# Optimization experiments

Hardware: AMD Instinct MI355X
Metric: run time of the kernel (lower is better)

Reference implementation:

```python
import jax, jax.numpy as jnp
import numpy as np

NUM_HEADS = 4
OUT_DIM = 64
IN_DIM = 128

def setup_inputs() -> dict:
    key = jax.random.key(0)
    k1, k2, k3, k4 = jax.random.split(key, 4)
    h = jax.random.normal(k1, (4, 256, IN_DIM), dtype=jnp.float32)
    adj = jax.random.randint(k2, (4, 256, 256), 0, 2).astype(jnp.int32)
    W = jax.random.normal(k3, (IN_DIM, NUM_HEADS * OUT_DIM), dtype=jnp.float32) * (1.0 / np.sqrt(IN_DIM))
    a = jax.random.normal(k4, (2 * OUT_DIM, 1), dtype=jnp.float32) * 0.1
    return {"h": h, "adj": adj, "W": W, "a": a}

def reference(h, adj, W, a):
    B, N, _ = h.shape
    H, D = NUM_HEADS, OUT_DIM
    Wh = (h @ W).reshape(B, N, H, D)                      # [B,N,H,D]
    # Exact replication of the torch repeat/view construction (row-major, same as torch.view)
    a1 = jnp.tile(Wh, (1, 1, 1, N)).reshape(B, N * H, N, D)
    a2 = jnp.tile(Wh, (1, N, 1, 1)).reshape(B, N * H, N, D)
    a_input = jnp.concatenate([a1, a2], axis=3)           # [B,N*H,N,2D]
    e = jax.nn.leaky_relu((a_input @ a)[..., 0], negative_slope=0.2)
    e = e.reshape(B, H, N, N)
    mask = adj[:, None, :, :] == 0                        # broadcast over heads
    attention = jax.nn.softmax(jnp.where(mask, -jnp.inf, e), axis=3)  # [B,H,N,N]
    h_prime = jnp.einsum('bhij,bjhd->bihd', attention, Wh)             # [B,N,H,D]
    return h_prime.reshape(B, N, H * D)
```

## Files before the change

kernel.cpp:

```cpp
#include <hip/hip_runtime.h>


typedef __attribute__((ext_vector_type(8))) short bf16x8;
typedef __attribute__((ext_vector_type(4))) float f32x4;

__device__ __forceinline__ short bf1(float x) {
  unsigned u = __builtin_bit_cast(unsigned, x);
  u = (u + 0x7FFFu + ((u >> 16) & 1u)) >> 16;
  return (short)u;
}
__device__ __forceinline__ bf16x8 pack8(float4 a, float4 b) {
  bf16x8 r;
  r[0]=bf1(a.x); r[1]=bf1(a.y); r[2]=bf1(a.z); r[3]=bf1(a.w);
  r[4]=bf1(b.x); r[5]=bf1(b.y); r[6]=bf1(b.z); r[7]=bf1(b.w);
  return r;
}

__global__ __launch_bounds__(512) void gat_prep(
    const float* __restrict__ h, const float* __restrict__ W,
    const float* __restrict__ a,
    short* __restrict__ WhT, float* __restrict__ f1g, float* __restrict__ f2g)
{
  const int tid  = threadIdx.x;
  const int lane = tid & 63;
  const int quad = lane >> 4, col = lane & 15;
  const int wv   = tid >> 6;
  const int blk  = blockIdx.x;
  const int nt = blk & 3, mt = (blk >> 2) & 3, b = blk >> 4;

  __shared__ short WbT[64][136];
  __shared__ float f1p[64][4];
  __shared__ float f2p[64][4];

#pragma unroll
  for (int q = 0; q < 4; q++) {
    const int idx = q * 512 + tid;
    const int k = idx >> 4, c4 = idx & 15;
    float4 w4 = *(const float4*)(W + k * 256 + nt * 64 + c4 * 4);
    WbT[c4*4 + 0][k] = bf1(w4.x);
    WbT[c4*4 + 1][k] = bf1(w4.y);
    WbT[c4*4 + 2][k] = bf1(w4.z);
    WbT[c4*4 + 3][k] = bf1(w4.w);
  }
  __syncthreads();

  const int tc = wv & 3;
  const float a1v = a[tc*16 + col];
  const float a2v = a[64 + tc*16 + col];

#pragma unroll
  for (int q = 0; q < 2; q++) {
    const int tr = (wv >> 2) * 2 + q;
    const float* hrow = h + (b*256 + mt*64 + tr*16 + col) * 128 + quad*8;
    f32x4 acc = {0.f, 0.f, 0.f, 0.f};
#pragma unroll
    for (int kk = 0; kk < 4; kk++) {
      float4 lo = *(const float4*)(hrow + kk*32);
      float4 hi = *(const float4*)(hrow + kk*32 + 4);
      bf16x8 bw = *(const bf16x8*)&WbT[tc*16 + col][kk*32 + quad*8];
      acc = __builtin_amdgcn_mfma_f32_16x16x32_bf16(pack8(lo, hi), bw, acc, 0, 0, 0);
    }
    {
      const int dcol = nt*64 + tc*16 + col;
      const int n0   = mt*64 + tr*16 + quad*4;
      int2 pk;
      pk.x = (int)((unsigned)(unsigned short)bf1(acc[0]) |
                   ((unsigned)(unsigned short)bf1(acc[1]) << 16));
      pk.y = (int)((unsigned)(unsigned short)bf1(acc[2]) |
                   ((unsigned)(unsigned short)bf1(acc[3]) << 16));
      *(int2*)(WhT + b*65536 + dcol*256 + n0) = pk;
    }
#pragma unroll
    for (int r = 0; r < 4; r++) {
      float v1 = acc[r] * a1v;
      float v2 = acc[r] * a2v;
#pragma unroll
      for (int off = 1; off < 16; off <<= 1) {
        v1 += __shfl_xor(v1, off, 64);
        v2 += __shfl_xor(v2, off, 64);
      }
      if (col == 0) {
        const int row = tr*16 + quad*4 + r;
        f1p[row][tc] = v1;
        f2p[row][tc] = v2;
      }
    }
  }
  __syncthreads();

  if (tid < 64) {
    const float s = f1p[tid][0] + f1p[tid][1] + f1p[tid][2] + f1p[tid][3];
    f1g[b*1024 + (mt*64 + tid)*4 + nt] = s;
  } else if (tid < 128) {
    const int n = tid - 64;
    const float s = f2p[n][0] + f2p[n][1] + f2p[n][2] + f2p[n][3];
    f2g[b*1024 + (mt*64 + n)*4 + nt] = s;
  }
}

__global__ __launch_bounds__(512) void gat_attn(
    const short* __restrict__ WhT, const float* __restrict__ f1g,
    const float* __restrict__ f2g, const int* __restrict__ adj,
    float* __restrict__ out)
{
  const int tid  = threadIdx.x;
  const int lane = tid & 63;
  const int quad = lane >> 4, col = lane & 15;
  const int wv   = tid >> 6;
  const int blk  = blockIdx.x;
  const int it2 = blk & 7, hp = (blk >> 3) & 3, b = blk >> 5;
  const int i0 = it2 * 32;

  __shared__ short attb[32][264];
  __shared__ float sinv[32];

#pragma unroll
  for (int rq = 0; rq < 4; rq++) {
    const int rr = wv*4 + rq;
    const int i  = i0 + rr;
    const float s1v = f1g[b*1024 + hp*256 + i];
    float4 f2v = *(const float4*)(f2g + b*1024 + (i & 3)*256 + lane*4);
    int4 av = *(const int4*)(adj + (b*256 + i)*256 + lane*4);
    float e0 = s1v + f2v.x, e1 = s1v + f2v.y, e2 = s1v + f2v.z, e3 = s1v + f2v.w;
    e0 = e0 > 0.f ? e0 : 0.2f*e0;  e1 = e1 > 0.f ? e1 : 0.2f*e1;
    e2 = e2 > 0.f ? e2 : 0.2f*e2;  e3 = e3 > 0.f ? e3 : 0.2f*e3;
    e0 = av.x ? e0 : -1e30f;  e1 = av.y ? e1 : -1e30f;
    e2 = av.z ? e2 : -1e30f;  e3 = av.w ? e3 : -1e30f;
    float m = fmaxf(fmaxf(e0, e1), fmaxf(e2, e3));
#pragma unroll
    for (int off = 32; off > 0; off >>= 1) m = fmaxf(m, __shfl_xor(m, off, 64));
    float x0 = __expf(e0 - m), x1 = __expf(e1 - m);
    float x2 = __expf(e2 - m), x3 = __expf(e3 - m);
    float s = (x0 + x1) + (x2 + x3);
    int2 pk2;
    pk2.x = (int)((unsigned)(unsigned short)bf1(x0) |
                  ((unsigned)(unsigned short)bf1(x1) << 16));
    pk2.y = (int)((unsigned)(unsigned short)bf1(x2) |
                  ((unsigned)(unsigned short)bf1(x3) << 16));
    *(int2*)&attb[rr][lane*4] = pk2;
#pragma unroll
    for (int off = 32; off > 0; off >>= 1) s += __shfl_xor(s, off, 64);
    if (lane == 0) sinv[rr] = 1.f / s;
  }
  __syncthreads();

  const int rt = wv >> 2, ct = wv & 3;
  bf16x8 af[8];
#pragma unroll
  for (int kk = 0; kk < 8; kk++)
    af[kk] = *(const bf16x8*)&attb[rt*16 + col][kk*32 + quad*8];
  const short* bp = WhT + b*65536 + (hp*64 + ct*16 + col)*256 + quad*8;
  f32x4 acc = {0.f, 0.f, 0.f, 0.f};
#pragma unroll
  for (int kk = 0; kk < 8; kk++) {
    bf16x8 bv = *(const bf16x8*)(bp + kk*32);
    acc = __builtin_amdgcn_mfma_f32_16x16x32_bf16(af[kk], bv, acc, 0, 0, 0);
  }
#pragma unroll
  for (int r = 0; r < 4; r++) {
    const int m = rt*16 + quad*4 + r;
    out[(b*256 + i0 + m)*256 + hp*64 + ct*16 + col] = acc[r] * sinv[m];
  }
}

extern "C" void kernel_launch(void* const* d_in, const int* in_sizes, int n_in,
                              void* d_out, int out_size, void* d_ws, size_t ws_size,
                              hipStream_t stream) {
  const float* h   = (const float*)d_in[0];
  const int*   adj = (const int*)d_in[1];
  const float* W   = (const float*)d_in[2];
  const float* a   = (const float*)d_in[3];
  float* out = (float*)d_out;

  short* WhT = (short*)d_ws;
  float* f1g = (float*)((char*)d_ws + 4*256*256*2);
  float* f2g = f1g + 4*1024;

  gat_prep<<<64, 512, 0, stream>>>(h, W, a, WhT, f1g, f2g);
  gat_attn<<<128, 512, 0, stream>>>(WhT, f1g, f2g, adj, out);
}
```

Before: 71.96 us.

## Prefetch attention operands, drop softmax max pass, and split prep grid finer

The attention kernel now issues all WhT, adj, f1 and f2 global loads at the start, so their latency overlaps the softmax work instead of stalling the MFMA loop afterwards. It also drops the row-max reduction from the softmax, exponentiating the raw logits directly. This saves a cross-lane shuffle pass per row but can overflow if a logit exceeds the float exp range. The prep kernel is split into twice as many blocks, each handling 32 rows, to spread the work over more CUs. The MFMA chain is also split into two independent accumulators to shorten the dependency chain.

Result: faster. 68.79 us (-4.4%).

```diff
diff --git a/kernel.cpp b/kernel.cpp
--- a/kernel.cpp
+++ b/kernel.cpp
@@ -26,11 +26,11 @@
   const int quad = lane >> 4, col = lane & 15;
   const int wv   = tid >> 6;
   const int blk  = blockIdx.x;
-  const int nt = blk & 3, mt = (blk >> 2) & 3, b = blk >> 4;
+  const int ms = blk & 7, nt = (blk >> 3) & 3, b = blk >> 5;
 
   __shared__ short WbT[64][136];
-  __shared__ float f1p[64][4];
-  __shared__ float f2p[64][4];
+  __shared__ float f1p[32][4];
+  __shared__ float f2p[32][4];
 
 #pragma unroll
   for (int q = 0; q < 4; q++) {
@@ -45,56 +45,53 @@
   __syncthreads();
 
   const int tc = wv & 3;
+  const int tr = wv >> 2;
   const float a1v = a[tc*16 + col];
   const float a2v = a[64 + tc*16 + col];
 
+  const float* hrow = h + (b*256 + ms*32 + tr*16 + col) * 128 + quad*8;
+  f32x4 acc = {0.f, 0.f, 0.f, 0.f};
 #pragma unroll
-  for (int q = 0; q < 2; q++) {
-    const int tr = (wv >> 2) * 2 + q;
-    const float* hrow = h + (b*256 + mt*64 + tr*16 + col) * 128 + quad*8;
-    f32x4 acc = {0.f, 0.f, 0.f, 0.f};
+  for (int kk = 0; kk < 4; kk++) {
+    float4 lo = *(const float4*)(hrow + kk*32);
+    float4 hi = *(const float4*)(hrow + kk*32 + 4);
+    bf16x8 bw = *(const bf16x8*)&WbT[tc*16 + col][kk*32 + quad*8];
+    acc = __builtin_amdgcn_mfma_f32_16x16x32_bf16(pack8(lo, hi), bw, acc, 0, 0, 0);
+  }
+  {
+    const int dcol = nt*64 + tc*16 + col;
+    const int n0   = ms*32 + tr*16 + quad*4;
+    int2 pk;
+    pk.x = (int)((unsigned)(unsigned short)bf1(acc[0]) |
+                 ((unsigned)(unsigned short)bf1(acc[1]) << 16));
+    pk.y = (int)((unsigned)(unsigned short)bf1(acc[2]) |
+                 ((unsigned)(unsigned short)bf1(acc[3]) << 16));
+    *(int2*)(WhT + b*65536 + dcol*256 + n0) = pk;
+  }
 #pragma unroll
-    for (int kk = 0; kk < 4; kk++) {
-      float4 lo = *(const float4*)(hrow + kk*32);
-      float4 hi = *(const float4*)(hrow + kk*32 + 4);
-      bf16x8 bw = *(const bf16x8*)&WbT[tc*16 + col][kk*32 + quad*8];
-      acc = __builtin_amdgcn_mfma_f32_16x16x32_bf16(pack8(lo, hi), bw, acc, 0, 0, 0);
+  for (int r = 0; r < 4; r++) {
+    float v1 = acc[r] * a1v;
+    float v2 = acc[r] * a2v;
+#pragma unroll
+    for (int off = 1; off < 16; off <<= 1) {
+      v1 += __shfl_xor(v1, off, 64);
+      v2 += __shfl_xor(v2, off, 64);
     }
-    {
-      const int dcol = nt*64 + tc*16 + col;
-      const int n0   = mt*64 + tr*16 + quad*4;
-      int2 pk;
-      pk.x = (int)((unsigned)(unsigned short)bf1(acc[0]) |
-                   ((unsigned)(unsigned short)bf1(acc[1]) << 16));
-      pk.y = (int)((unsigned)(unsigned short)bf1(acc[2]) |
-                   ((unsigned)(unsigned short)bf1(acc[3]) << 16));
-      *(int2*)(WhT + b*65536 + dcol*256 + n0) = pk;
-    }
-#pragma unroll
-    for (int r = 0; r < 4; r++) {
-      float v1 = acc[r] * a1v;
-      float v2 = acc[r] * a2v;
-#pragma unroll
-      for (int off = 1; off < 16; off <<= 1) {
-        v1 += __shfl_xor(v1, off, 64);
-        v2 += __shfl_xor(v2, off, 64);
-      }
-      if (col == 0) {
-        const int row = tr*16 + quad*4 + r;
-        f1p[row][tc] = v1;
-        f2p[row][tc] = v2;
-      }
+    if (col == 0) {
+      const int row = tr*16 + quad*4 + r;
+      f1p[row][tc] = v1;
+      f2p[row][tc] = v2;
     }
   }
   __syncthreads();
 
-  if (tid < 64) {
+  if (tid < 32) {
     const float s = f1p[tid][0] + f1p[tid][1] + f1p[tid][2] + f1p[tid][3];
-    f1g[b*1024 + (mt*64 + tid)*4 + nt] = s;
-  } else if (tid < 128) {
+    f1g[b*1024 + (ms*32 + tid)*4 + nt] = s;
+  } else if (tid >= 64 && tid < 96) {
     const int n = tid - 64;
     const float s = f2p[n][0] + f2p[n][1] + f2p[n][2] + f2p[n][3];
-    f2g[b*1024 + (mt*64 + n)*4 + nt] = s;
+    f2g[b*1024 + (ms*32 + n)*4 + nt] = s;
   }
 }
 
@@ -114,52 +111,63 @@
   __shared__ short attb[32][264];
   __shared__ float sinv[32];
 
+  const int rt = wv >> 2, ct = wv & 3;
+
+  bf16x8 bv[8];
+  const short* bp = WhT + b*65536 + (hp*64 + ct*16 + col)*256 + quad*8;
+#pragma unroll
+  for (int kk = 0; kk < 8; kk++) bv[kk] = *(const bf16x8*)(bp + kk*32);
+
+  float4 f2v[4]; int4 av[4]; float f1s[4];
+#pragma unroll
+  for (int rq = 0; rq < 4; rq++) {
+    const int i = i0 + wv*4 + rq;
+    f2v[rq] = *(const float4*)(f2g + b*1024 + rq*256 + lane*4);
+    av[rq]  = *(const int4*)(adj + (b*256 + i)*256 + lane*4);
+    f1s[rq] = f1g[b*1024 + hp*256 + i];
+  }
+
 #pragma unroll
   for (int rq = 0; rq < 4; rq++) {
     const int rr = wv*4 + rq;
-    const int i  = i0 + rr;
-    const float s1v = f1g[b*1024 + hp*256 + i];
-    float4 f2v = *(const float4*)(f2g + b*1024 + (i & 3)*256 + lane*4);
-    int4 av = *(const int4*)(adj + (b*256 + i)*256 + lane*4);
-    float e0 = s1v + f2v.x, e1 = s1v + f2v.y, e2 = s1v + f2v.z, e3 = s1v + f2v.w;
+    const float s1v = f1s[rq];
+    float e0 = s1v + f2v[rq].x, e1 = s1v + f2v[rq].y;
+    float e2 = s1v + f2v[rq].z, e3 = s1v + f2v[rq].w;
     e0 = e0 > 0.f ? e0 : 0.2f*e0;  e1 = e1 > 0.f ? e1 : 0.2f*e1;
     e2 = e2 > 0.f ? e2 : 0.2f*e2;  e3 = e3 > 0.f ? e3 : 0.2f*e3;
-    e0 = av.x ? e0 : -1e30f;  e1 = av.y ? e1 : -1e30f;
-    e2 = av.z ? e2 : -1e30f;  e3 = av.w ? e3 : -1e30f;
-    float m = fmaxf(fmaxf(e0, e1), fmaxf(e2, e3));
-#pragma unroll
-    for (int off = 32; off > 0; off >>= 1) m = fmaxf(m, __shfl_xor(m, off, 64));
-    float x0 = __expf(e0 - m), x1 = __expf(e1 - m);
-    float x2 = __expf(e2 - m), x3 = __expf(e3 - m);
-    float s = (x0 + x1) + (x2 + x3);
+    e0 = av[rq].x ? e0 : -1e30f;  e1 = av[rq].y ? e1 : -1e30f;
+    e2 = av[rq].z ? e2 : -1e30f;  e3 = av[rq].w ? e3 : -1e30f;
+    float x0 = __expf(e0), x1 = __expf(e1);
+    float x2 = __expf(e2), x3 = __expf(e3);
     int2 pk2;
     pk2.x = (int)((unsigned)(unsigned short)bf1(x0) |
                   ((unsigned)(unsigned short)bf1(x1) << 16));
     pk2.y = (int)((unsigned)(unsigned short)bf1(x2) |
                   ((unsigned)(unsigned short)bf1(x3) << 16));
     *(int2*)&attb[rr][lane*4] = pk2;
+    float s = (x0 + x1) + (x2 + x3);
 #pragma unroll
     for (int off = 32; off > 0; off >>= 1) s += __shfl_xor(s, off, 64);
     if (lane == 0) sinv[rr] = 1.f / s;
   }
   __syncthreads();
 
-  const int rt = wv >> 2, ct = wv & 3;
   bf16x8 af[8];
 #pragma unroll
   for (int kk = 0; kk < 8; kk++)
     af[kk] = *(const bf16x8*)&attb[rt*16 + col][kk*32 + quad*8];
-  const short* bp = WhT + b*65536 + (hp*64 + ct*16 + col)*256 + quad*8;
-  f32x4 acc = {0.f, 0.f, 0.f, 0.f};
+  f32x4 acc0 = {0.f, 0.f, 0.f, 0.f};
+  f32x4 acc1 = {0.f, 0.f, 0.f, 0.f};
 #pragma unroll
-  for (int kk = 0; kk < 8; kk++) {
-    bf16x8 bv = *(const bf16x8*)(bp + kk*32);
-    acc = __builtin_amdgcn_mfma_f32_16x16x32_bf16(af[kk], bv, acc, 0, 0, 0);
-  }
+  for (int kk = 0; kk < 4; kk++)
+    acc0 = __builtin_amdgcn_mfma_f32_16x16x32_bf16(af[kk], bv[kk], acc0, 0, 0, 0);
+#pragma unroll
+  for (int kk = 4; kk < 8; kk++)
+    acc1 = __builtin_amdgcn_mfma_f32_16x16x32_bf16(af[kk], bv[kk], acc1, 0, 0, 0);
 #pragma unroll
   for (int r = 0; r < 4; r++) {
     const int m = rt*16 + quad*4 + r;
-    out[(b*256 + i0 + m)*256 + hp*64 + ct*16 + col] = acc[r] * sinv[m];
+    out[(b*256 + i0 + m)*256 + hp*64 + ct*16 + col] = (acc0[r] + acc1[r]) * sinv[m];
   }
 }
 
@@ -176,6 +184,6 @@
   float* f1g = (float*)((char*)d_ws + 4*256*256*2);
   float* f2g = f1g + 4*1024;
 
-  gat_prep<<<64, 512, 0, stream>>>(h, W, a, WhT, f1g, f2g);
+  gat_prep<<<128, 512, 0, stream>>>(h, W, a, WhT, f1g, f2g);
   gat_attn<<<128, 512, 0, stream>>>(WhT, f1g, f2g, adj, out);
 }
```
